# Optimization experiments

Hardware: AMD Instinct MI355X
Metric: run time of the kernel (lower is better)

The kernel has to match this reference:

```python
import jax, jax.numpy as jnp
import numpy as np

N = 8192
F_IN = 256
F_OUT = 128
NEG_BIG = -9.0e15


def setup_inputs() -> dict:
    key = jax.random.key(0)
    k1, k2, k3, k4 = jax.random.split(key, 4)
    x = jax.random.normal(k1, (N, F_IN), dtype=jnp.float32)
    W = jax.random.normal(k2, (F_IN, F_OUT), dtype=jnp.float32) * 0.05
    a = jax.random.normal(k3, (2 * F_OUT, 1), dtype=jnp.float32) * 0.05
    adj = jax.random.randint(k4, (N, N), 0, 2, dtype=jnp.int32)
    return {"x": x, "W": W, "a": a, "adj": adj}


def reference(x, W, a, adj):
    # h = x @ W : [N, F_OUT]
    h = x @ W
    # Original builds [N, N, 2F] concat then matmuls with a. Since
    # a_input[i,j] = concat(h_i, h_j), the score is separable:
    # (a_input @ a)[i,j] = h_i . a[:F] + h_j . a[F:]
    a1 = a[:F_OUT, 0]   # [F_OUT]
    a2 = a[F_OUT:, 0]   # [F_OUT]
    s1 = h @ a1         # [N]
    s2 = h @ a2         # [N]
    e = jax.nn.leaky_relu(s1[:, None] + s2[None, :], negative_slope=0.2)
    e = jnp.where(adj > 0, e, jnp.float32(NEG_BIG))
    attention = jax.nn.softmax(e, axis=1)   # [N, N]
    h_prime = attention @ h                 # [N, F_OUT]
    return jax.nn.elu(h_prime)
```

## Files before the change

kernel.cpp:

```cpp
#include <hip/hip_runtime.h>
#include <math.h>

#define NN 8192

typedef __attribute__((ext_vector_type(8))) short short8;
typedef __attribute__((ext_vector_type(4))) short short4v;
typedef __attribute__((ext_vector_type(4))) float f32x4;
typedef __attribute__((ext_vector_type(4))) int int4v;

#define L2E 1.4426950408889634f

typedef __attribute__((address_space(3))) unsigned lds_u32;
typedef __attribute__((address_space(1))) unsigned g_u32;

__device__ __forceinline__ void gll16(const void* g, void* l) {
    __builtin_amdgcn_global_load_lds((const g_u32*)g, (lds_u32*)l, 16, 0, 0);
}

__device__ __forceinline__ short f2bf(float f) {
    union { float f; unsigned u; } v; v.f = f;
    unsigned r = v.u + 0x7fffu + ((v.u >> 16) & 1u);
    return (short)(r >> 16);
}

__device__ __forceinline__ f32x4 zero4() {
    f32x4 v; v[0] = 0.f; v[1] = 0.f; v[2] = 0.f; v[3] = 0.f; return v;
}

__global__ void k0_wt(const float* __restrict__ W, short* __restrict__ WT) {
    int idx = blockIdx.x * 256 + threadIdx.x;
    if (idx < 256 * 128) {
        int k = idx & 255;
        int f = idx >> 8;
        WT[f * 256 + k] = f2bf(W[k * 128 + f]);
    }
}

__global__ __launch_bounds__(128) void k1_h(
        const float* __restrict__ x, const short* __restrict__ WT,
        const float* __restrict__ a, short* __restrict__ hT,
        float* __restrict__ s1L2E, float* __restrict__ s2L2E) {
    const int w = threadIdx.x >> 6;
    const int l = threadIdx.x & 63;
    const int quad = l >> 4;
    const int fr = l & 15;
    const int i0 = blockIdx.x * 32 + w * 16;

    f32x4 acc[8];
#pragma unroll
    for (int t = 0; t < 8; ++t) acc[t] = zero4();

    const float* xrow = x + (size_t)(i0 + fr) * 256;
#pragma unroll
    for (int kk = 0; kk < 8; ++kk) {
        const int k0 = kk * 32 + quad * 8;
        f32x4 xa = *(const f32x4*)(xrow + k0);
        f32x4 xb = *(const f32x4*)(xrow + k0 + 4);
        short8 av;
#pragma unroll
        for (int e = 0; e < 4; ++e) { av[e] = f2bf(xa[e]); av[4 + e] = f2bf(xb[e]); }
#pragma unroll
        for (int t = 0; t < 8; ++t) {
            short8 bv = *(const short8*)(WT + (t * 16 + fr) * 256 + k0);
            acc[t] = __builtin_amdgcn_mfma_f32_16x16x32_bf16(av, bv, acc[t], 0, 0, 0);
        }
    }

    float s1p[4] = {0.f, 0.f, 0.f, 0.f};
    float s2p[4] = {0.f, 0.f, 0.f, 0.f};
#pragma unroll
    for (int t = 0; t < 8; ++t) {
        float a1v = a[t * 16 + fr];
        float a2v = a[128 + t * 16 + fr];
#pragma unroll
        for (int r = 0; r < 4; ++r) {
            s1p[r] += acc[t][r] * a1v;
            s2p[r] += acc[t][r] * a2v;
        }
    }
#pragma unroll
    for (int r = 0; r < 4; ++r) {
#pragma unroll
        for (int m = 1; m < 16; m <<= 1) {
            s1p[r] += __shfl_xor(s1p[r], m, 64);
            s2p[r] += __shfl_xor(s2p[r], m, 64);
        }
    }
    if (fr == 0) {
#pragma unroll
        for (int r = 0; r < 4; ++r) {
            const int i = i0 + quad * 4 + r;
            s1L2E[i] = s1p[r] * L2E;
            s2L2E[i] = s2p[r] * L2E;
        }
    }

#pragma unroll
    for (int t = 0; t < 8; ++t) {
        short4v hv;
#pragma unroll
        for (int r = 0; r < 4; ++r) hv[r] = f2bf(acc[t][r]);
        *(short4v*)(hT + (size_t)(t * 16 + fr) * NN + i0 + quad * 4) = hv;
    }
}

template<int JSPLIT, bool PARTIAL>
__global__ __launch_bounds__(256, 3) void k2_attn(
        const int* __restrict__ adj, const short* __restrict__ hT,
        const float* __restrict__ s1g, const float* __restrict__ s2g,
        float* __restrict__ pvp, float* __restrict__ zp,
        float* __restrict__ out) {
    constexpr int JW = NN / JSPLIT;
    constexpr int NSTEP = JW / 64;
    constexpr int BUFB = 25600;
    __shared__ __align__(16) char lds_c[2 * BUFB + 256];

    const int tid = threadIdx.x;
    const int w = tid >> 6;
    const int l = tid & 63;
    const int quad = l >> 4;
    const int fr = l & 15;
    const int rh = w >> 1;
    const int wj = w & 1;
    const int rb = blockIdx.x / JSPLIT;
    const int jb = blockIdx.x % JSPLIT;
    const int r32 = rb * 32;
    const int jbb = jb * JW;

    const float S = s1g[r32 + rh * 16 + fr];

    const char* hsrc[4];
    {
        const char* hbase = (const char*)hT;
#pragma unroll
        for (int p = 0; p < 4; ++p) {
            const int o = p * 4096 + tid * 16;
            const int row = o >> 7;
            const int colb = o & 127;
            hsrc[p] = hbase + (size_t)row * (NN * 2) + (size_t)jbb * 2
                    + (colb ^ ((row & 7) << 4));
        }
    }
    const char* asrc[2];
    {
        const char* abase = (const char*)adj;
#pragma unroll
        for (int p = 0; p < 2; ++p) {
            const int o = p * 4096 + tid * 16;
            const int row = o >> 8;
            const int colb = o & 255;
            asrc[p] = abase + (size_t)(r32 + row) * (NN * 4) + (size_t)jbb * 4
                    + (colb ^ ((row & 7) << 4));
        }
    }
    const char* csrc = (const char*)s2g + (size_t)jbb * 4 + l * 16;

    auto STAGE = [&](int jt, int buf) {
        jt = (jt < NSTEP) ? jt : NSTEP - 1;
        char* hd = lds_c + buf * BUFB + w * 1024;
        char* ad = lds_c + buf * BUFB + 16384 + w * 1024;
        char* cd = lds_c + buf * BUFB + 24576;
        const size_t hof = (size_t)jt * 128;
        const size_t aof = (size_t)jt * 256;
#pragma unroll
        for (int p = 0; p < 4; ++p) gll16(hsrc[p] + hof, hd + p * 4096);
#pragma unroll
        for (int p = 0; p < 2; ++p) gll16(asrc[p] + aof, ad + p * 4096);
        gll16(csrc + aof, cd);
    };

    f32x4 acc[8];
#pragma unroll
    for (int t = 0; t < 8; ++t) acc[t] = zero4();
    float zacc = 0.f;

    STAGE(0, 0); STAGE(1, 1);

    for (int t = 0; t < NSTEP; ++t) {
        const int cur = t & 1;
        asm volatile("s_waitcnt vmcnt(7)" ::: "memory");
        __builtin_amdgcn_s_barrier();
        __builtin_amdgcn_sched_barrier(0);
        __builtin_amdgcn_s_setprio(1);

        const char* hb = lds_c + cur * BUFB;
        const char* ab = lds_c + cur * BUFB + 16384;
        const float* cb = (const float*)(lds_c + cur * BUFB + 24576);

        const int arow = rh * 16 + fr;
        const unsigned aswz = (unsigned)((arow & 7) << 4);
        const unsigned al = (unsigned)(arow * 256 + wj * 128 + quad * 32);
        const int4v g0 = *(const int4v*)(ab + (al ^ aswz));
        const int4v g1 = *(const int4v*)(ab + ((al + 16) ^ aswz));
        const f32x4 c0 = *(const f32x4*)(cb + wj * 32 + quad * 8);
        const f32x4 c1 = *(const f32x4*)(cb + wj * 32 + quad * 8 + 4);

        short8 pa;
        {
            float zs = 0.f;
#pragma unroll
            for (int e = 0; e < 8; ++e) {
                const float cv = (e < 4) ? c0[e & 3] : c1[e & 3];
                const int gv = (e < 4) ? g0[e & 3] : g1[e & 3];
                const float u = S + cv;
                const float tt = fmaxf(u, 0.2f * u);
                const float p = (gv > 0) ? exp2f(tt) : 0.f;
                zs += p;
                pa[e] = f2bf(p);
            }
            zacc += zs;
        }

#pragma unroll
        for (int t8 = 0; t8 < 8; ++t8) {
            const int hrow = t8 * 16 + fr;
            const short8 bv = *(const short8*)(
                hb + ((unsigned)(hrow * 128 + wj * 64 + quad * 16) ^ ((hrow & 7) << 4)));
            acc[t8] = __builtin_amdgcn_mfma_f32_16x16x32_bf16(pa, bv, acc[t8], 0, 0, 0);
        }

        __builtin_amdgcn_s_setprio(0);
        __builtin_amdgcn_sched_barrier(0);
        asm volatile("" ::: "memory");
        __builtin_amdgcn_s_barrier();

        STAGE(t + 2, cur);
    }

    asm volatile("s_waitcnt vmcnt(0)" ::: "memory");
    __syncthreads();

    zacc += __shfl_xor(zacc, 16, 64);
    zacc += __shfl_xor(zacc, 32, 64);
    float* zb = (float*)(lds_c + 2 * BUFB);
    if (l < 16) zb[w * 16 + l] = zacc;

    float* red = (float*)lds_c;
    if (wj == 1) {
#pragma unroll
        for (int t = 0; t < 8; ++t)
            *(f32x4*)(red + rh * 2048 + t * 256 + l * 4) = acc[t];
    }
    __syncthreads();

    if (wj == 0) {
#pragma unroll
        for (int t = 0; t < 8; ++t)
            acc[t] += *(const f32x4*)(red + rh * 2048 + t * 256 + l * 4);
#pragma unroll
        for (int r = 0; r < 4; ++r) {
            const int irow = quad * 4 + r;
            const float z = zb[rh * 32 + irow] + zb[rh * 32 + 16 + irow];
            const int grow = r32 + rh * 16 + irow;
            if (PARTIAL) {
                if (fr == 0) zp[(size_t)jb * NN + grow] = z;
                float* orow = pvp + ((size_t)jb * NN + grow) * 128;
#pragma unroll
                for (int t = 0; t < 8; ++t) orow[t * 16 + fr] = acc[t][r];
            } else {
                const float inv = 1.0f / z;
                float* orow = out + (size_t)grow * 128;
#pragma unroll
                for (int t = 0; t < 8; ++t) {
                    float v = acc[t][r] * inv;
                    orow[t * 16 + fr] = (v > 0.f) ? v : expm1f(v);
                }
            }
        }
    }
}

__global__ __launch_bounds__(256) void k3_fin(
        const float* __restrict__ pvp, const float* __restrict__ zp,
        float* __restrict__ out, int jsplit) {
    const int idx = blockIdx.x * 256 + threadIdx.x;
    const int row = idx >> 5;
    const int c = (idx & 31) << 2;
    f32x4 s = zero4();
    float z = 0.f;
    for (int p = 0; p < jsplit; ++p) {
        s += *(const f32x4*)(pvp + ((size_t)p * NN + row) * 128 + c);
        z += zp[(size_t)p * NN + row];
    }
    const float inv = 1.0f / z;
    f32x4 o;
#pragma unroll
    for (int e = 0; e < 4; ++e) {
        float v = s[e] * inv;
        o[e] = (v > 0.f) ? v : expm1f(v);
    }
    *(f32x4*)(out + (size_t)row * 128 + c) = o;
}

extern "C" void kernel_launch(void* const* d_in, const int* in_sizes, int n_in,
                              void* d_out, int out_size, void* d_ws, size_t ws_size,
                              hipStream_t stream) {
    const float* x   = (const float*)d_in[0];
    const float* W   = (const float*)d_in[1];
    const float* a   = (const float*)d_in[2];
    const int*   adj = (const int*)d_in[3];
    float* out = (float*)d_out;

    char* ws = (char*)d_ws;
    const size_t MB = 1024 * 1024;
    short* hT    = (short*)ws;
    float* s1L2E = (float*)(ws + 2 * MB);
    float* s2L2E = (float*)(ws + 2 * MB + 32768);
    short* WT    = (short*)(ws + 2 * MB + 65536);
    const size_t base = 2 * MB + 131072;

    auto need = [&](size_t js) {
        return base + js * ((size_t)NN * 128 * 4) + js * ((size_t)NN * 4);
    };
    int jsplit;
    if (ws_size >= need(4)) jsplit = 4;
    else if (ws_size >= need(2)) jsplit = 2;
    else if (ws_size >= need(1)) jsplit = 1;
    else jsplit = 0;

    float* pvp = (float*)(ws + base);
    float* zp  = (float*)(ws + base + (size_t)(jsplit > 0 ? jsplit : 1) * NN * 128 * 4);

    k0_wt<<<128, 256, 0, stream>>>(W, WT);
    k1_h<<<256, 128, 0, stream>>>(x, WT, a, hT, s1L2E, s2L2E);

    if (jsplit == 4) {
        k2_attn<4, true><<<1024, 256, 0, stream>>>(adj, hT, s1L2E, s2L2E, pvp, zp, nullptr);
        k3_fin<<<1024, 256, 0, stream>>>(pvp, zp, out, 4);
    } else if (jsplit == 2) {
        k2_attn<2, true><<<512, 256, 0, stream>>>(adj, hT, s1L2E, s2L2E, pvp, zp, nullptr);
        k3_fin<<<1024, 256, 0, stream>>>(pvp, zp, out, 2);
    } else if (jsplit == 1) {
        k2_attn<1, true><<<256, 256, 0, stream>>>(adj, hT, s1L2E, s2L2E, pvp, zp, nullptr);
        k3_fin<<<1024, 256, 0, stream>>>(pvp, zp, out, 1);
    } else {
        k2_attn<1, false><<<256, 256, 0, stream>>>(adj, hT, s1L2E, s2L2E, nullptr, nullptr, out);
    }
}
```

Measured before the change: 102.2 us.

## Pack adjacency into bitmask and restructure attention kernel around direct register loads

Adds a pre-pass that compresses the int32 adjacency matrix into a 1-bit-per-entry mask via wave ballots. The attention kernel then reads 64-bit mask words instead of int32 rows. The kernel drops its LDS double-buffered pipeline and loads h and s2 straight into registers, with each wave computing two 16-row tiles over its own column slice and a cross-wave reduction at the end. The full adjacency read still happens in the pack kernel, and the separate launch plus the extra mask write and read add traffic. Removing LDS staging may expose global load latency.

Result: slower. 189.2 us (+85.1%).

```diff
diff --git a/kernel.cpp b/kernel.cpp
--- a/kernel.cpp
+++ b/kernel.cpp
@@ -6,16 +6,8 @@
 typedef __attribute__((ext_vector_type(8))) short short8;
 typedef __attribute__((ext_vector_type(4))) short short4v;
 typedef __attribute__((ext_vector_type(4))) float f32x4;
-typedef __attribute__((ext_vector_type(4))) int int4v;
 
 #define L2E 1.4426950408889634f
-
-typedef __attribute__((address_space(3))) unsigned lds_u32;
-typedef __attribute__((address_space(1))) unsigned g_u32;
-
-__device__ __forceinline__ void gll16(const void* g, void* l) {
-    __builtin_amdgcn_global_load_lds((const g_u32*)g, (lds_u32*)l, 16, 0, 0);
-}
 
 __device__ __forceinline__ short f2bf(float f) {
     union { float f; unsigned u; } v; v.f = f;
@@ -33,6 +25,19 @@
         int k = idx & 255;
         int f = idx >> 8;
         WT[f * 256 + k] = f2bf(W[k * 128 + f]);
+    }
+}
+
+__global__ __launch_bounds__(256) void k_pack(
+        const int* __restrict__ adj, unsigned long long* __restrict__ bm) {
+    const int l = threadIdx.x & 63;
+    const size_t wid = (size_t)blockIdx.x * 4 + (threadIdx.x >> 6);
+    const size_t nw = (size_t)gridDim.x * 4;
+    const size_t NWORDS = (size_t)NN * NN / 64;
+    for (size_t m = wid; m < NWORDS; m += nw) {
+        const int v = adj[m * 64 + l];
+        const unsigned long long mask = __ballot(v > 0);
+        if (l == 0) bm[m] = mask;
     }
 }
 
@@ -106,164 +111,136 @@
 
 template<int JSPLIT, bool PARTIAL>
 __global__ __launch_bounds__(256, 3) void k2_attn(
-        const int* __restrict__ adj, const short* __restrict__ hT,
+        const unsigned long long* __restrict__ bm, const short* __restrict__ hT,
         const float* __restrict__ s1g, const float* __restrict__ s2g,
         float* __restrict__ pvp, float* __restrict__ zp,
         float* __restrict__ out) {
     constexpr int JW = NN / JSPLIT;
-    constexpr int NSTEP = JW / 64;
-    constexpr int BUFB = 25600;
-    __shared__ __align__(16) char lds_c[2 * BUFB + 256];
+    constexpr int NSTEP = JW / 128;
+    __shared__ __align__(16) char lds_c[16384 + 512];
 
     const int tid = threadIdx.x;
     const int w = tid >> 6;
     const int l = tid & 63;
     const int quad = l >> 4;
     const int fr = l & 15;
-    const int rh = w >> 1;
-    const int wj = w & 1;
-    const int rb = blockIdx.x / JSPLIT;
+    const int r32 = (blockIdx.x / JSPLIT) * 32;
     const int jb = blockIdx.x % JSPLIT;
-    const int r32 = rb * 32;
     const int jbb = jb * JW;
 
-    const float S = s1g[r32 + rh * 16 + fr];
-
-    const char* hsrc[4];
-    {
-        const char* hbase = (const char*)hT;
-#pragma unroll
-        for (int p = 0; p < 4; ++p) {
-            const int o = p * 4096 + tid * 16;
-            const int row = o >> 7;
-            const int colb = o & 127;
-            hsrc[p] = hbase + (size_t)row * (NN * 2) + (size_t)jbb * 2
-                    + (colb ^ ((row & 7) << 4));
-        }
-    }
-    const char* asrc[2];
-    {
-        const char* abase = (const char*)adj;
-#pragma unroll
-        for (int p = 0; p < 2; ++p) {
-            const int o = p * 4096 + tid * 16;
-            const int row = o >> 8;
-            const int colb = o & 255;
-            asrc[p] = abase + (size_t)(r32 + row) * (NN * 4) + (size_t)jbb * 4
-                    + (colb ^ ((row & 7) << 4));
-        }
-    }
-    const char* csrc = (const char*)s2g + (size_t)jbb * 4 + l * 16;
-
-    auto STAGE = [&](int jt, int buf) {
-        jt = (jt < NSTEP) ? jt : NSTEP - 1;
-        char* hd = lds_c + buf * BUFB + w * 1024;
-        char* ad = lds_c + buf * BUFB + 16384 + w * 1024;
-        char* cd = lds_c + buf * BUFB + 24576;
-        const size_t hof = (size_t)jt * 128;
-        const size_t aof = (size_t)jt * 256;
-#pragma unroll
-        for (int p = 0; p < 4; ++p) gll16(hsrc[p] + hof, hd + p * 4096);
-#pragma unroll
-        for (int p = 0; p < 2; ++p) gll16(asrc[p] + aof, ad + p * 4096);
-        gll16(csrc + aof, cd);
-    };
-
-    f32x4 acc[8];
-#pragma unroll
-    for (int t = 0; t < 8; ++t) acc[t] = zero4();
-    float zacc = 0.f;
-
-    STAGE(0, 0); STAGE(1, 1);
+    const float S0 = s1g[r32 + fr];
+    const float S1 = s1g[r32 + 16 + fr];
+
+    const unsigned long long* bw0 = bm + (size_t)(r32 + fr) * (NN / 64)
+                                  + (jbb / 64) + (w >> 1);
+    const unsigned long long* bw1 = bw0 + (size_t)16 * (NN / 64);
+    const int bsh = (w & 1) * 32 + quad * 8;
+
+    const short* hbase = hT + (size_t)fr * NN + jbb + w * 32 + quad * 8;
+    const float* cbase = s2g + jbb + w * 32 + quad * 8;
+
+    f32x4 acc[2][8];
+#pragma unroll
+    for (int m = 0; m < 2; ++m)
+#pragma unroll
+        for (int t = 0; t < 8; ++t) acc[m][t] = zero4();
+    float zacc0 = 0.f, zacc1 = 0.f;
 
     for (int t = 0; t < NSTEP; ++t) {
-        const int cur = t & 1;
-        asm volatile("s_waitcnt vmcnt(7)" ::: "memory");
-        __builtin_amdgcn_s_barrier();
-        __builtin_amdgcn_sched_barrier(0);
-        __builtin_amdgcn_s_setprio(1);
-
-        const char* hb = lds_c + cur * BUFB;
-        const char* ab = lds_c + cur * BUFB + 16384;
-        const float* cb = (const float*)(lds_c + cur * BUFB + 24576);
-
-        const int arow = rh * 16 + fr;
-        const unsigned aswz = (unsigned)((arow & 7) << 4);
-        const unsigned al = (unsigned)(arow * 256 + wj * 128 + quad * 32);
-        const int4v g0 = *(const int4v*)(ab + (al ^ aswz));
-        const int4v g1 = *(const int4v*)(ab + ((al + 16) ^ aswz));
-        const f32x4 c0 = *(const f32x4*)(cb + wj * 32 + quad * 8);
-        const f32x4 c1 = *(const f32x4*)(cb + wj * 32 + quad * 8 + 4);
-
-        short8 pa;
+        const int jo = t * 128;
+
+        const unsigned long long b0 = bw0[t * 2];
+        const unsigned long long b1 = bw1[t * 2];
+        const f32x4 c0 = *(const f32x4*)(cbase + jo);
+        const f32x4 c1 = *(const f32x4*)(cbase + jo + 4);
+        short8 bv[8];
+#pragma unroll
+        for (int F = 0; F < 8; ++F)
+            bv[F] = *(const short8*)(hbase + (size_t)F * 16 * NN + jo);
+
+        const unsigned bb0 = (unsigned)(b0 >> bsh) & 0xffu;
+        const unsigned bb1 = (unsigned)(b1 >> bsh) & 0xffu;
+
+        short8 pa0, pa1;
         {
-            float zs = 0.f;
+            float zs0 = 0.f, zs1 = 0.f;
 #pragma unroll
             for (int e = 0; e < 8; ++e) {
-                const float cv = (e < 4) ? c0[e & 3] : c1[e & 3];
-                const int gv = (e < 4) ? g0[e & 3] : g1[e & 3];
-                const float u = S + cv;
-                const float tt = fmaxf(u, 0.2f * u);
-                const float p = (gv > 0) ? exp2f(tt) : 0.f;
-                zs += p;
-                pa[e] = f2bf(p);
+                const float cv = (e < 4) ? c0[e] : c1[e - 4];
+                const float u0 = S0 + cv;
+                const float u1 = S1 + cv;
+                const float t0 = fmaxf(u0, 0.2f * u0);
+                const float t1 = fmaxf(u1, 0.2f * u1);
+                const float p0 = ((bb0 >> e) & 1u) ? exp2f(t0) : 0.f;
+                const float p1 = ((bb1 >> e) & 1u) ? exp2f(t1) : 0.f;
+                zs0 += p0; zs1 += p1;
+                pa0[e] = f2bf(p0);
+                pa1[e] = f2bf(p1);
             }
-            zacc += zs;
-        }
-
-#pragma unroll
-        for (int t8 = 0; t8 < 8; ++t8) {
-            const int hrow = t8 * 16 + fr;
-            const short8 bv = *(const short8*)(
-                hb + ((unsigned)(hrow * 128 + wj * 64 + quad * 16) ^ ((hrow & 7) << 4)));
-            acc[t8] = __builtin_amdgcn_mfma_f32_16x16x32_bf16(pa, bv, acc[t8], 0, 0, 0);
-        }
-
-        __builtin_amdgcn_s_setprio(0);
-        __builtin_amdgcn_sched_barrier(0);
-        asm volatile("" ::: "memory");
-        __builtin_amdgcn_s_barrier();
-
-        STAGE(t + 2, cur);
-    }
-
-    asm volatile("s_waitcnt vmcnt(0)" ::: "memory");
-    __syncthreads();
-
-    zacc += __shfl_xor(zacc, 16, 64);
-    zacc += __shfl_xor(zacc, 32, 64);
-    float* zb = (float*)(lds_c + 2 * BUFB);
-    if (l < 16) zb[w * 16 + l] = zacc;
-
+            zacc0 += zs0; zacc1 += zs1;
+        }
+
+#pragma unroll
+        for (int F = 0; F < 8; ++F) {
+            acc[0][F] = __builtin_amdgcn_mfma_f32_16x16x32_bf16(pa0, bv[F], acc[0][F], 0, 0, 0);
+            acc[1][F] = __builtin_amdgcn_mfma_f32_16x16x32_bf16(pa1, bv[F], acc[1][F], 0, 0, 0);
+        }
+    }
+
+    zacc0 += __shfl_xor(zacc0, 16, 64);
+    zacc0 += __shfl_xor(zacc0, 32, 64);
+    zacc1 += __shfl_xor(zacc1, 16, 64);
+    zacc1 += __shfl_xor(zacc1, 32, 64);
     float* red = (float*)lds_c;
-    if (wj == 1) {
-#pragma unroll
-        for (int t = 0; t < 8; ++t)
-            *(f32x4*)(red + rh * 2048 + t * 256 + l * 4) = acc[t];
-    }
-    __syncthreads();
-
-    if (wj == 0) {
-#pragma unroll
-        for (int t = 0; t < 8; ++t)
-            acc[t] += *(const f32x4*)(red + rh * 2048 + t * 256 + l * 4);
-#pragma unroll
-        for (int r = 0; r < 4; ++r) {
-            const int irow = quad * 4 + r;
-            const float z = zb[rh * 32 + irow] + zb[rh * 32 + 16 + irow];
-            const int grow = r32 + rh * 16 + irow;
-            if (PARTIAL) {
-                if (fr == 0) zp[(size_t)jb * NN + grow] = z;
-                float* orow = pvp + ((size_t)jb * NN + grow) * 128;
-#pragma unroll
-                for (int t = 0; t < 8; ++t) orow[t * 16 + fr] = acc[t][r];
-            } else {
-                const float inv = 1.0f / z;
-                float* orow = out + (size_t)grow * 128;
-#pragma unroll
-                for (int t = 0; t < 8; ++t) {
-                    float v = acc[t][r] * inv;
-                    orow[t * 16 + fr] = (v > 0.f) ? v : expm1f(v);
+    float* zb = (float*)(lds_c + 16384);
+    if (l < 16) {
+        zb[w * 32 + l] = zacc0;
+        zb[w * 32 + 16 + l] = zacc1;
+    }
+
+#pragma unroll
+    for (int ww = 1; ww < 4; ++ww) {
+        if (w == ww) {
+#pragma unroll
+            for (int m = 0; m < 2; ++m)
+#pragma unroll
+                for (int t = 0; t < 8; ++t)
+                    *(f32x4*)(red + ((m * 8 + t) * 64 + l) * 4) = acc[m][t];
+        }
+        __syncthreads();
+        if (w == 0) {
+#pragma unroll
+            for (int m = 0; m < 2; ++m)
+#pragma unroll
+                for (int t = 0; t < 8; ++t)
+                    acc[m][t] += *(const f32x4*)(red + ((m * 8 + t) * 64 + l) * 4);
+        }
+        __syncthreads();
+    }
+
+    if (w == 0) {
+#pragma unroll
+        for (int m = 0; m < 2; ++m) {
+#pragma unroll
+            for (int r = 0; r < 4; ++r) {
+                const int irow = m * 16 + quad * 4 + r;
+                float z = 0.f;
+#pragma unroll
+                for (int ww = 0; ww < 4; ++ww) z += zb[ww * 32 + irow];
+                const int grow = r32 + irow;
+                if (PARTIAL) {
+                    if (fr == 0) zp[(size_t)jb * NN + grow] = z;
+                    float* orow = pvp + ((size_t)jb * NN + grow) * 128;
+#pragma unroll
+                    for (int t = 0; t < 8; ++t) orow[t * 16 + fr] = acc[m][t][r];
+                } else {
+                    const float inv = 1.0f / z;
+                    float* orow = out + (size_t)grow * 128;
+#pragma unroll
+                    for (int t = 0; t < 8; ++t) {
+                        float v = acc[m][t][r] * inv;
+                        orow[t * 16 + fr] = (v > 0.f) ? v : expm1f(v);
+                    }
                 }
             }
         }
@@ -307,7 +284,8 @@
     float* s1L2E = (float*)(ws + 2 * MB);
     float* s2L2E = (float*)(ws + 2 * MB + 32768);
     short* WT    = (short*)(ws + 2 * MB + 65536);
-    const size_t base = 2 * MB + 131072;
+    unsigned long long* bmp = (unsigned long long*)(ws + 2 * MB + 131072);
+    const size_t base = 2 * MB + 131072 + (size_t)NN * NN / 8;
 
     auto need = [&](size_t js) {
         return base + js * ((size_t)NN * 128 * 4) + js * ((size_t)NN * 4);
@@ -323,17 +301,18 @@
 
     k0_wt<<<128, 256, 0, stream>>>(W, WT);
     k1_h<<<256, 128, 0, stream>>>(x, WT, a, hT, s1L2E, s2L2E);
+    k_pack<<<2048, 256, 0, stream>>>(adj, bmp);
 
     if (jsplit == 4) {
-        k2_attn<4, true><<<1024, 256, 0, stream>>>(adj, hT, s1L2E, s2L2E, pvp, zp, nullptr);
+        k2_attn<4, true><<<1024, 256, 0, stream>>>(bmp, hT, s1L2E, s2L2E, pvp, zp, nullptr);
         k3_fin<<<1024, 256, 0, stream>>>(pvp, zp, out, 4);
     } else if (jsplit == 2) {
-        k2_attn<2, true><<<512, 256, 0, stream>>>(adj, hT, s1L2E, s2L2E, pvp, zp, nullptr);
+        k2_attn<2, true><<<512, 256, 0, stream>>>(bmp, hT, s1L2E, s2L2E, pvp, zp, nullptr);
         k3_fin<<<1024, 256, 0, stream>>>(pvp, zp, out, 2);
     } else if (jsplit == 1) {
-        k2_attn<1, true><<<256, 256, 0, stream>>>(adj, hT, s1L2E, s2L2E, pvp, zp, nullptr);
+        k2_attn<1, true><<<256, 256, 0, stream>>>(bmp, hT, s1L2E, s2L2E, pvp, zp, nullptr);
         k3_fin<<<1024, 256, 0, stream>>>(pvp, zp, out, 1);
     } else {
-        k2_attn<1, false><<<256, 256, 0, stream>>>(adj, hT, s1L2E, s2L2E, nullptr, nullptr, out);
-    }
-}
+        k2_attn<1, false><<<256, 256, 0, stream>>>(bmp, hT, s1L2E, s2L2E, nullptr, nullptr, out);
+    }
+}
```

## Preload adjacency as LDS bitmask before main loop, single-buffer h staging

Applied to the files above, without the earlier changes.

Instead of streaming int32 adjacency tiles through LDS in each loop step, the kernel now reads all of a block's adjacency rows up front, packs each group of four entries into a 4-bit nibble, and stores them as a swizzled bitmask in LDS. The main loop then stages only h and s2 tiles, prefetching one step ahead and synchronising with a plain __syncthreads. This shrinks per-step LDS traffic and instruction count. In exchange, all adjacency loads happen in a prologue that does not overlap with MFMA work, and the prefetch depth drops from two steps to one.

Result: slower. 122.2 us (+19.6%).

```diff
diff --git a/kernel.cpp b/kernel.cpp
--- a/kernel.cpp
+++ b/kernel.cpp
@@ -112,8 +112,8 @@
         float* __restrict__ out) {
     constexpr int JW = NN / JSPLIT;
     constexpr int NSTEP = JW / 64;
-    constexpr int BUFB = 25600;
-    __shared__ __align__(16) char lds_c[2 * BUFB + 256];
+    constexpr int NCH = JW / 256;
+    __shared__ __align__(16) char lds_c[51456];
 
     const int tid = threadIdx.x;
     const int w = tid >> 6;
@@ -141,57 +141,60 @@
                     + (colb ^ ((row & 7) << 4));
         }
     }
-    const char* asrc[2];
+    const char* csrc = (const char*)s2g + (size_t)jbb * 4 + l * 16;
+
+    auto STAGE = [&](int jt, int buf) {
+        char* hd = lds_c + 16384 + buf * 16384 + w * 1024;
+        char* cd = lds_c + 49152 + buf * 1024;
+        const size_t hof = (size_t)jt * 128;
+#pragma unroll
+        for (int p = 0; p < 4; ++p) gll16(hsrc[p] + hof, hd + p * 4096);
+        gll16(csrc + (size_t)jt * 256, cd);
+    };
+
+    STAGE(0, 0);
+
     {
         const char* abase = (const char*)adj;
-#pragma unroll
-        for (int p = 0; p < 2; ++p) {
-            const int o = p * 4096 + tid * 16;
-            const int row = o >> 8;
-            const int colb = o & 255;
-            asrc[p] = abase + (size_t)(r32 + row) * (NN * 4) + (size_t)jbb * 4
-                    + (colb ^ ((row & 7) << 4));
-        }
-    }
-    const char* csrc = (const char*)s2g + (size_t)jbb * 4 + l * 16;
-
-    auto STAGE = [&](int jt, int buf) {
-        jt = (jt < NSTEP) ? jt : NSTEP - 1;
-        char* hd = lds_c + buf * BUFB + w * 1024;
-        char* ad = lds_c + buf * BUFB + 16384 + w * 1024;
-        char* cd = lds_c + buf * BUFB + 24576;
-        const size_t hof = (size_t)jt * 128;
-        const size_t aof = (size_t)jt * 256;
-#pragma unroll
-        for (int p = 0; p < 4; ++p) gll16(hsrc[p] + hof, hd + p * 4096);
-#pragma unroll
-        for (int p = 0; p < 2; ++p) gll16(asrc[p] + aof, ad + p * 4096);
-        gll16(csrc + aof, cd);
-    };
+        for (int c = 0; c < NCH; ++c) {
+            int4v v[8];
+#pragma unroll
+            for (int p = 0; p < 8; ++p) {
+                const int r = w * 8 + p;
+                v[p] = *(const int4v*)(abase + (size_t)(r32 + r) * (NN * 4)
+                                     + (size_t)(jbb + c * 256) * 4 + l * 16);
+            }
+#pragma unroll
+            for (int p = 0; p < 8; ++p) {
+                const int r = w * 8 + p;
+                const unsigned nib = (v[p][0] > 0 ? 1u : 0u) | (v[p][1] > 0 ? 2u : 0u)
+                                   | (v[p][2] > 0 ? 4u : 0u) | (v[p][3] > 0 ? 8u : 0u);
+                const int logical = c * 64 + l;
+                lds_c[r * 512 + (logical ^ ((r & 7) << 6))] = (char)nib;
+            }
+        }
+    }
+    __syncthreads();
 
     f32x4 acc[8];
 #pragma unroll
     for (int t = 0; t < 8; ++t) acc[t] = zero4();
     float zacc = 0.f;
 
-    STAGE(0, 0); STAGE(1, 1);
-
+    const int arow = rh * 16 + fr;
+    const unsigned bswz = (unsigned)((arow & 7) << 6);
+
+    int cur = 0;
     for (int t = 0; t < NSTEP; ++t) {
-        const int cur = t & 1;
-        asm volatile("s_waitcnt vmcnt(7)" ::: "memory");
-        __builtin_amdgcn_s_barrier();
+        if (t + 1 < NSTEP) STAGE(t + 1, cur ^ 1);
         __builtin_amdgcn_sched_barrier(0);
-        __builtin_amdgcn_s_setprio(1);
-
-        const char* hb = lds_c + cur * BUFB;
-        const char* ab = lds_c + cur * BUFB + 16384;
-        const float* cb = (const float*)(lds_c + cur * BUFB + 24576);
-
-        const int arow = rh * 16 + fr;
-        const unsigned aswz = (unsigned)((arow & 7) << 4);
-        const unsigned al = (unsigned)(arow * 256 + wj * 128 + quad * 32);
-        const int4v g0 = *(const int4v*)(ab + (al ^ aswz));
-        const int4v g1 = *(const int4v*)(ab + ((al + 16) ^ aswz));
+
+        const char* hb = lds_c + 16384 + cur * 16384;
+        const float* cb = (const float*)(lds_c + 49152 + cur * 1024);
+
+        const unsigned blog = (unsigned)(t * 16 + wj * 8 + quad * 2);
+        const unsigned bits = *(const unsigned short*)(lds_c + arow * 512 + (blog ^ bswz));
+
         const f32x4 c0 = *(const f32x4*)(cb + wj * 32 + quad * 8);
         const f32x4 c1 = *(const f32x4*)(cb + wj * 32 + quad * 8 + 4);
 
@@ -200,11 +203,11 @@
             float zs = 0.f;
 #pragma unroll
             for (int e = 0; e < 8; ++e) {
-                const float cv = (e < 4) ? c0[e & 3] : c1[e & 3];
-                const int gv = (e < 4) ? g0[e & 3] : g1[e & 3];
+                const float cv = (e < 4) ? c0[e] : c1[e - 4];
+                const unsigned bit = (bits >> ((e >> 2) * 8 + (e & 3))) & 1u;
                 const float u = S + cv;
                 const float tt = fmaxf(u, 0.2f * u);
-                const float p = (gv > 0) ? exp2f(tt) : 0.f;
+                const float p = bit ? exp2f(tt) : 0.f;
                 zs += p;
                 pa[e] = f2bf(p);
             }
@@ -219,23 +222,16 @@
             acc[t8] = __builtin_amdgcn_mfma_f32_16x16x32_bf16(pa, bv, acc[t8], 0, 0, 0);
         }
 
-        __builtin_amdgcn_s_setprio(0);
-        __builtin_amdgcn_sched_barrier(0);
-        asm volatile("" ::: "memory");
-        __builtin_amdgcn_s_barrier();
-
-        STAGE(t + 2, cur);
-    }
-
-    asm volatile("s_waitcnt vmcnt(0)" ::: "memory");
-    __syncthreads();
+        __syncthreads();
+        cur ^= 1;
+    }
 
     zacc += __shfl_xor(zacc, 16, 64);
     zacc += __shfl_xor(zacc, 32, 64);
-    float* zb = (float*)(lds_c + 2 * BUFB);
+    float* zb = (float*)(lds_c + 51200);
     if (l < 16) zb[w * 16 + l] = zacc;
 
-    float* red = (float*)lds_c;
+    float* red = (float*)(lds_c + 16384);
     if (wj == 1) {
 #pragma unroll
         for (int t = 0; t < 8; ++t)
```

## Double attention row tile to 64 rows per block to reuse staged h

Applied to the files above, without the earlier changes.

Each attention block now covers 64 query rows instead of 32. Every wave computes two 16-row MFMA tiles that share the same h B-fragment loaded from LDS, so hT traffic per row is halved and LDS reads are amortised. The change also enlarges the LDS buffers, lowers launch bounds to two blocks per CU, halves the grid sizes and drops the setprio hints. In exchange it doubles accumulator registers and LDS use, and with half as many blocks occupancy and wave parallelism could suffer on the 256-CU part.

New measurement: 83.91 us. 17.9% less time.

```diff
diff --git a/kernel.cpp b/kernel.cpp
--- a/kernel.cpp
+++ b/kernel.cpp
@@ -105,15 +105,15 @@
 }
 
 template<int JSPLIT, bool PARTIAL>
-__global__ __launch_bounds__(256, 3) void k2_attn(
+__global__ __launch_bounds__(256, 2) void k2_attn(
         const int* __restrict__ adj, const short* __restrict__ hT,
         const float* __restrict__ s1g, const float* __restrict__ s2g,
         float* __restrict__ pvp, float* __restrict__ zp,
         float* __restrict__ out) {
     constexpr int JW = NN / JSPLIT;
     constexpr int NSTEP = JW / 64;
-    constexpr int BUFB = 25600;
-    __shared__ __align__(16) char lds_c[2 * BUFB + 256];
+    constexpr int BUFB = 33792;
+    __shared__ __align__(16) char lds_c[2 * BUFB + 512];
 
     const int tid = threadIdx.x;
     const int w = tid >> 6;
@@ -124,91 +124,101 @@
     const int wj = w & 1;
     const int rb = blockIdx.x / JSPLIT;
     const int jb = blockIdx.x % JSPLIT;
-    const int r32 = rb * 32;
+    const int r64 = rb * 64;
     const int jbb = jb * JW;
 
-    const float S = s1g[r32 + rh * 16 + fr];
+    const float S0 = s1g[r64 + rh * 32 + fr];
+    const float S1 = s1g[r64 + rh * 32 + 16 + fr];
 
     const char* hsrc[4];
+    const char* asrc[4];
     {
         const char* hbase = (const char*)hT;
+        const char* abase = (const char*)adj;
 #pragma unroll
         for (int p = 0; p < 4; ++p) {
-            const int o = p * 4096 + tid * 16;
-            const int row = o >> 7;
-            const int colb = o & 127;
-            hsrc[p] = hbase + (size_t)row * (NN * 2) + (size_t)jbb * 2
-                    + (colb ^ ((row & 7) << 4));
-        }
-    }
-    const char* asrc[2];
-    {
-        const char* abase = (const char*)adj;
-#pragma unroll
-        for (int p = 0; p < 2; ++p) {
-            const int o = p * 4096 + tid * 16;
-            const int row = o >> 8;
-            const int colb = o & 255;
-            asrc[p] = abase + (size_t)(r32 + row) * (NN * 4) + (size_t)jbb * 4
-                    + (colb ^ ((row & 7) << 4));
+            const int off = w * 4096 + p * 1024 + l * 16;
+            {
+                const int row = off >> 7;
+                const int colb = off & 127;
+                hsrc[p] = hbase + (size_t)row * (NN * 2) + (size_t)jbb * 2
+                        + (colb ^ ((row & 7) << 4));
+            }
+            {
+                const int row = off >> 8;
+                const int colb = off & 255;
+                asrc[p] = abase + (size_t)(r64 + row) * (NN * 4) + (size_t)jbb * 4
+                        + (colb ^ ((row & 7) << 4));
+            }
         }
     }
     const char* csrc = (const char*)s2g + (size_t)jbb * 4 + l * 16;
 
     auto STAGE = [&](int jt, int buf) {
         jt = (jt < NSTEP) ? jt : NSTEP - 1;
-        char* hd = lds_c + buf * BUFB + w * 1024;
-        char* ad = lds_c + buf * BUFB + 16384 + w * 1024;
-        char* cd = lds_c + buf * BUFB + 24576;
+        char* hd = lds_c + buf * BUFB + w * 4096;
+        char* ad = lds_c + buf * BUFB + 16384 + w * 4096;
+        char* cd = lds_c + buf * BUFB + 32768;
         const size_t hof = (size_t)jt * 128;
         const size_t aof = (size_t)jt * 256;
 #pragma unroll
-        for (int p = 0; p < 4; ++p) gll16(hsrc[p] + hof, hd + p * 4096);
-#pragma unroll
-        for (int p = 0; p < 2; ++p) gll16(asrc[p] + aof, ad + p * 4096);
+        for (int p = 0; p < 4; ++p) gll16(hsrc[p] + hof, hd + p * 1024);
+#pragma unroll
+        for (int p = 0; p < 4; ++p) gll16(asrc[p] + aof, ad + p * 1024);
         gll16(csrc + aof, cd);
     };
 
-    f32x4 acc[8];
-#pragma unroll
-    for (int t = 0; t < 8; ++t) acc[t] = zero4();
-    float zacc = 0.f;
+    f32x4 acc[2][8];
+#pragma unroll
+    for (int m = 0; m < 2; ++m)
+#pragma unroll
+        for (int t = 0; t < 8; ++t) acc[m][t] = zero4();
+    float zacc0 = 0.f, zacc1 = 0.f;
 
     STAGE(0, 0); STAGE(1, 1);
+
+    const int ar0 = rh * 32 + fr;
+    const int ar1 = rh * 32 + 16 + fr;
+    const unsigned aswz = (unsigned)((ar0 & 7) << 4);
+    const unsigned a0 = (unsigned)(ar0 * 256 + wj * 128 + quad * 32);
+    const unsigned a1 = (unsigned)(ar1 * 256 + wj * 128 + quad * 32);
 
     for (int t = 0; t < NSTEP; ++t) {
         const int cur = t & 1;
-        asm volatile("s_waitcnt vmcnt(7)" ::: "memory");
+        asm volatile("s_waitcnt vmcnt(9)" ::: "memory");
         __builtin_amdgcn_s_barrier();
         __builtin_amdgcn_sched_barrier(0);
-        __builtin_amdgcn_s_setprio(1);
 
         const char* hb = lds_c + cur * BUFB;
         const char* ab = lds_c + cur * BUFB + 16384;
-        const float* cb = (const float*)(lds_c + cur * BUFB + 24576);
-
-        const int arow = rh * 16 + fr;
-        const unsigned aswz = (unsigned)((arow & 7) << 4);
-        const unsigned al = (unsigned)(arow * 256 + wj * 128 + quad * 32);
-        const int4v g0 = *(const int4v*)(ab + (al ^ aswz));
-        const int4v g1 = *(const int4v*)(ab + ((al + 16) ^ aswz));
-        const f32x4 c0 = *(const f32x4*)(cb + wj * 32 + quad * 8);
-        const f32x4 c1 = *(const f32x4*)(cb + wj * 32 + quad * 8 + 4);
-
-        short8 pa;
+        const float* cb = (const float*)(lds_c + cur * BUFB + 32768);
+
+        const int4v g00 = *(const int4v*)(ab + (a0 ^ aswz));
+        const int4v g01 = *(const int4v*)(ab + ((a0 + 16) ^ aswz));
+        const int4v g10 = *(const int4v*)(ab + (a1 ^ aswz));
+        const int4v g11 = *(const int4v*)(ab + ((a1 + 16) ^ aswz));
+        const f32x4 c0 = *(const f32x4*)((const char*)cb + wj * 128 + quad * 32);
+        const f32x4 c1 = *(const f32x4*)((const char*)cb + wj * 128 + quad * 32 + 16);
+
+        short8 pa0, pa1;
         {
-            float zs = 0.f;
+            float zs0 = 0.f, zs1 = 0.f;
 #pragma unroll
             for (int e = 0; e < 8; ++e) {
-                const float cv = (e < 4) ? c0[e & 3] : c1[e & 3];
-                const int gv = (e < 4) ? g0[e & 3] : g1[e & 3];
-                const float u = S + cv;
-                const float tt = fmaxf(u, 0.2f * u);
-                const float p = (gv > 0) ? exp2f(tt) : 0.f;
-                zs += p;
-                pa[e] = f2bf(p);
+                const float cv = (e < 4) ? c0[e] : c1[e - 4];
+                const int gv0 = (e < 4) ? g00[e] : g01[e - 4];
+                const int gv1 = (e < 4) ? g10[e] : g11[e - 4];
+                const float u0 = S0 + cv;
+                const float u1 = S1 + cv;
+                const float t0 = fmaxf(u0, 0.2f * u0);
+                const float t1 = fmaxf(u1, 0.2f * u1);
+                const float p0 = (gv0 > 0) ? exp2f(t0) : 0.f;
+                const float p1 = (gv1 > 0) ? exp2f(t1) : 0.f;
+                zs0 += p0; zs1 += p1;
+                pa0[e] = f2bf(p0);
+                pa1[e] = f2bf(p1);
             }
-            zacc += zs;
+            zacc0 += zs0; zacc1 += zs1;
         }
 
 #pragma unroll
@@ -216,54 +226,64 @@
             const int hrow = t8 * 16 + fr;
             const short8 bv = *(const short8*)(
                 hb + ((unsigned)(hrow * 128 + wj * 64 + quad * 16) ^ ((hrow & 7) << 4)));
-            acc[t8] = __builtin_amdgcn_mfma_f32_16x16x32_bf16(pa, bv, acc[t8], 0, 0, 0);
-        }
-
-        __builtin_amdgcn_s_setprio(0);
+            acc[0][t8] = __builtin_amdgcn_mfma_f32_16x16x32_bf16(pa0, bv, acc[0][t8], 0, 0, 0);
+            acc[1][t8] = __builtin_amdgcn_mfma_f32_16x16x32_bf16(pa1, bv, acc[1][t8], 0, 0, 0);
+        }
+
         __builtin_amdgcn_sched_barrier(0);
-        asm volatile("" ::: "memory");
         __builtin_amdgcn_s_barrier();
-
         STAGE(t + 2, cur);
     }
 
     asm volatile("s_waitcnt vmcnt(0)" ::: "memory");
     __syncthreads();
 
-    zacc += __shfl_xor(zacc, 16, 64);
-    zacc += __shfl_xor(zacc, 32, 64);
+    zacc0 += __shfl_xor(zacc0, 16, 64);
+    zacc0 += __shfl_xor(zacc0, 32, 64);
+    zacc1 += __shfl_xor(zacc1, 16, 64);
+    zacc1 += __shfl_xor(zacc1, 32, 64);
     float* zb = (float*)(lds_c + 2 * BUFB);
-    if (l < 16) zb[w * 16 + l] = zacc;
+    if (l < 16) {
+        zb[w * 32 + l] = zacc0;
+        zb[w * 32 + 16 + l] = zacc1;
+    }
 
     float* red = (float*)lds_c;
     if (wj == 1) {
 #pragma unroll
-        for (int t = 0; t < 8; ++t)
-            *(f32x4*)(red + rh * 2048 + t * 256 + l * 4) = acc[t];
+        for (int m = 0; m < 2; ++m)
+#pragma unroll
+            for (int t8 = 0; t8 < 8; ++t8)
+                *(f32x4*)(red + rh * 4096 + (m * 8 + t8) * 256 + l * 4) = acc[m][t8];
     }
     __syncthreads();
 
     if (wj == 0) {
 #pragma unroll
-        for (int t = 0; t < 8; ++t)
-            acc[t] += *(const f32x4*)(red + rh * 2048 + t * 256 + l * 4);
-#pragma unroll
-        for (int r = 0; r < 4; ++r) {
-            const int irow = quad * 4 + r;
-            const float z = zb[rh * 32 + irow] + zb[rh * 32 + 16 + irow];
-            const int grow = r32 + rh * 16 + irow;
-            if (PARTIAL) {
-                if (fr == 0) zp[(size_t)jb * NN + grow] = z;
-                float* orow = pvp + ((size_t)jb * NN + grow) * 128;
-#pragma unroll
-                for (int t = 0; t < 8; ++t) orow[t * 16 + fr] = acc[t][r];
-            } else {
-                const float inv = 1.0f / z;
-                float* orow = out + (size_t)grow * 128;
-#pragma unroll
-                for (int t = 0; t < 8; ++t) {
-                    float v = acc[t][r] * inv;
-                    orow[t * 16 + fr] = (v > 0.f) ? v : expm1f(v);
+        for (int m = 0; m < 2; ++m)
+#pragma unroll
+            for (int t8 = 0; t8 < 8; ++t8)
+                acc[m][t8] += *(const f32x4*)(red + rh * 4096 + (m * 8 + t8) * 256 + l * 4);
+#pragma unroll
+        for (int m = 0; m < 2; ++m) {
+#pragma unroll
+            for (int r = 0; r < 4; ++r) {
+                const int rr = m * 16 + quad * 4 + r;
+                const float z = zb[(rh * 2 + 0) * 32 + rr] + zb[(rh * 2 + 1) * 32 + rr];
+                const int grow = r64 + rh * 32 + rr;
+                if (PARTIAL) {
+                    if (fr == 0) zp[(size_t)jb * NN + grow] = z;
+                    float* orow = pvp + ((size_t)jb * NN + grow) * 128;
+#pragma unroll
+                    for (int t8 = 0; t8 < 8; ++t8) orow[t8 * 16 + fr] = acc[m][t8][r];
+                } else {
+                    const float inv = 1.0f / z;
+                    float* orow = out + (size_t)grow * 128;
+#pragma unroll
+                    for (int t8 = 0; t8 < 8; ++t8) {
+                        float v = acc[m][t8][r] * inv;
+                        orow[t8 * 16 + fr] = (v > 0.f) ? v : expm1f(v);
+                    }
                 }
             }
         }
@@ -325,15 +345,15 @@
     k1_h<<<256, 128, 0, stream>>>(x, WT, a, hT, s1L2E, s2L2E);
 
     if (jsplit == 4) {
-        k2_attn<4, true><<<1024, 256, 0, stream>>>(adj, hT, s1L2E, s2L2E, pvp, zp, nullptr);
+        k2_attn<4, true><<<512, 256, 0, stream>>>(adj, hT, s1L2E, s2L2E, pvp, zp, nullptr);
         k3_fin<<<1024, 256, 0, stream>>>(pvp, zp, out, 4);
     } else if (jsplit == 2) {
-        k2_attn<2, true><<<512, 256, 0, stream>>>(adj, hT, s1L2E, s2L2E, pvp, zp, nullptr);
+        k2_attn<2, true><<<256, 256, 0, stream>>>(adj, hT, s1L2E, s2L2E, pvp, zp, nullptr);
         k3_fin<<<1024, 256, 0, stream>>>(pvp, zp, out, 2);
     } else if (jsplit == 1) {
-        k2_attn<1, true><<<256, 256, 0, stream>>>(adj, hT, s1L2E, s2L2E, pvp, zp, nullptr);
+        k2_attn<1, true><<<128, 256, 0, stream>>>(adj, hT, s1L2E, s2L2E, pvp, zp, nullptr);
         k3_fin<<<1024, 256, 0, stream>>>(pvp, zp, out, 1);
     } else {
-        k2_attn<1, false><<<256, 256, 0, stream>>>(adj, hT, s1L2E, s2L2E, nullptr, nullptr, out);
-    }
-}
+        k2_attn<1, false><<<128, 256, 0, stream>>>(adj, hT, s1L2E, s2L2E, nullptr, nullptr, out);
+    }
+}
```
